# Optimization experiments

Measured on AMD Instinct MI355X. Metric: run time of the kernel, lower is better.

Reference implementation:

```python
import jax, jax.numpy as jnp
import numpy as np

GROUPS = 32
EPS = 1e-5
NUM_HEADS = 8


def group_norm(x, w, b):
    # x: (B, C, H, W)
    B, C, H, W = x.shape
    xg = x.reshape(B, GROUPS, C // GROUPS, H, W)
    mean = xg.mean(axis=(2, 3, 4), keepdims=True)
    var = xg.var(axis=(2, 3, 4), keepdims=True)
    xg = (xg - mean) * jax.lax.rsqrt(var + EPS)
    x = xg.reshape(B, C, H, W)
    return x * w[None, :, None, None] + b[None, :, None, None]


def setup_inputs() -> dict:
    key = jax.random.key(0)
    ks = jax.random.split(key, 4)
    B, C, H, W = 16, 512, 32, 32
    x = jax.random.normal(ks[0], (B, C, H, W), dtype=jnp.float32)
    gn_w = jnp.ones((C,), dtype=jnp.float32)
    gn_b = jnp.zeros((C,), dtype=jnp.float32)
    qkv_w = jax.random.normal(ks[1], (3 * C, C), dtype=jnp.float32) * 0.02  # 1x1 conv, no bias
    proj_w = jax.random.normal(ks[2], (C, C), dtype=jnp.float32) * 0.02     # 1x1 conv
    proj_b = jax.random.normal(ks[3], (C,), dtype=jnp.float32) * 0.02
    return {"x": x, "gn_w": gn_w, "gn_b": gn_b, "qkv_w": qkv_w,
            "proj_w": proj_w, "proj_b": proj_b}


def reference(x, gn_w, gn_b, qkv_w, proj_w, proj_b):
    B, C, H, W = x.shape
    heads = NUM_HEADS
    head_dim = C // heads
    HW = H * W
    scale = 1.0 / (head_dim ** 0.5)

    x = group_norm(x, gn_w, gn_b)  # residual uses the NORMED x, matching source

    qkv = jnp.einsum('bchw,oc->bohw', x, qkv_w)                     # (B, 3C, H, W)
    qkv = qkv.reshape(B, 3, heads, head_dim, HW)
    q, k, v = qkv[:, 0], qkv[:, 1], qkv[:, 2]                       # (B, heads, head_dim, HW)

    # Replicate the source's exact permute(0,2,3,1)+reshape (scrambles semantics, but faithful)
    def to_bmh(t):
        return jnp.transpose(t, (0, 2, 3, 1)).reshape(B * heads, HW, head_dim)
    q, k, v = to_bmh(q), to_bmh(k), to_bmh(v)

    attn = jax.nn.softmax(jnp.einsum('bnd,bmd->bnm', q, k) * scale, axis=-1)  # (B*heads, HW, HW)
    h = jnp.einsum('bnm,bmd->bnd', attn, v)                                   # (B*heads, HW, head_dim)

    h = h.reshape(B, heads, H, W, head_dim)
    h = jnp.transpose(h, (0, 1, 4, 2, 3)).reshape(B, C, H, W)

    out = jnp.einsum('bchw,oc->bohw', h, proj_w) + proj_b[None, :, None, None]
    return out + x
```

## Files before the change

kernel.cpp:

```cpp
#include <hip/hip_runtime.h>
#include <stdint.h>

typedef unsigned short u16;
typedef short bfrag __attribute__((ext_vector_type(8)));
typedef float ffrag __attribute__((ext_vector_type(4)));
typedef u16 us4 __attribute__((ext_vector_type(4)));
typedef uint32_t u32x4 __attribute__((ext_vector_type(4)));

#define HW 1024
#define C_DIM 512
#define O3 1536
#define BATCH 16

__device__ __forceinline__ u16 f2bf(float f) {
    uint32_t u = __builtin_bit_cast(uint32_t, f);
    u += 0x7FFFu + ((u >> 16) & 1u);
    return (u16)(u >> 16);
}
__device__ __forceinline__ float bf2f(u16 v) {
    return __builtin_bit_cast(float, (uint32_t)v << 16);
}
__device__ __forceinline__ float fexp2(float x) { return __builtin_amdgcn_exp2f(x); }
__device__ __forceinline__ void async16(const u16* src, u16* ldsDst) {
    __builtin_amdgcn_global_load_lds(
        (const __attribute__((address_space(1))) uint32_t*)src,
        (__attribute__((address_space(3))) uint32_t*)ldsDst, 16, 0, 0);
}

__global__ __launch_bounds__(256) void gn_cvt_kernel(
    const float* __restrict__ x, const float* __restrict__ gw, const float* __restrict__ gb,
    u16* __restrict__ xgt,
    const float* __restrict__ qkvw, u16* __restrict__ qkvwb,
    const float* __restrict__ projw, u16* __restrict__ projwb)
{
    __shared__ u16 tile[16 * 1032];
    __shared__ float red[8];
    const int tid = threadIdx.x;
    if (blockIdx.x >= 512) {
        int i = (blockIdx.x - 512) * 256 + tid;
        if (i < 196608) {
            float4 v = ((const float4*)qkvw)[i];
            us4 o = { f2bf(v.x), f2bf(v.y), f2bf(v.z), f2bf(v.w) };
            ((us4*)qkvwb)[i] = o;
        } else {
            int j = i - 196608;
            float4 v = ((const float4*)projw)[j];
            us4 o = { f2bf(v.x), f2bf(v.y), f2bf(v.z), f2bf(v.w) };
            ((us4*)projwb)[j] = o;
        }
        return;
    }
    const int batch = blockIdx.x >> 5, g = blockIdx.x & 31;
    const float* xp = x + ((size_t)batch * C_DIM + g * 16) * HW;

    float s = 0.f, ss = 0.f;
#pragma unroll
    for (int it = 0; it < 16; ++it) {
        int i4 = it * 256 + tid;
        float4 v = ((const float4*)xp)[i4];
        int ci = i4 >> 8;
        int hw = (i4 & 255) * 4;
        s += v.x + v.y + v.z + v.w;
        ss += v.x * v.x + v.y * v.y + v.z * v.z + v.w * v.w;
        us4 u = { f2bf(v.x), f2bf(v.y), f2bf(v.z), f2bf(v.w) };
        *(us4*)&tile[ci * 1032 + hw] = u;
    }
#pragma unroll
    for (int m = 1; m <= 32; m <<= 1) { s += __shfl_xor(s, m, 64); ss += __shfl_xor(ss, m, 64); }
    if ((tid & 63) == 0) { red[tid >> 6] = s; red[4 + (tid >> 6)] = ss; }
    __syncthreads();
    float S = red[0] + red[1] + red[2] + red[3];
    float SS = red[4] + red[5] + red[6] + red[7];
    const float mean = S * (1.f / 16384.f);
    const float istd = rsqrtf(SS * (1.f / 16384.f) - mean * mean + 1e-5f);

    u16* xtp = xgt + (size_t)batch * HW * C_DIM + g * 16;
#pragma unroll
    for (int it = 0; it < 16; ++it) {
        int hw = (tid >> 2) + it * 64;
        int c0 = (tid & 3) * 4;
        us4 o;
#pragma unroll
        for (int k2 = 0; k2 < 4; ++k2) {
            int ci = c0 + k2;
            float sc = gw[g * 16 + ci] * istd;
            float bi = gb[g * 16 + ci] - mean * sc;
            o[k2] = f2bf(bf2f(tile[ci * 1032 + hw]) * sc + bi);
        }
        *(us4*)&xtp[(size_t)hw * C_DIM + c0] = o;
    }
}

__global__ __launch_bounds__(256) void qkv_gemm_kernel(
    const u16* __restrict__ A, const u16* __restrict__ B, u16* __restrict__ Out,
    u16* __restrict__ vtout)
{
    __shared__ __align__(16) u16 smem[32768];
    const int tid = threadIdx.x;
    const int l = tid & 63, w = tid >> 6;
    const int swz = (blockIdx.x & 7) * 192 + (blockIdx.x >> 3);
    const int batch = swz / 96, t = swz % 96;
    const int tm = t / 12, tn = t % 12;
    A += (size_t)batch * (HW * C_DIM) + (size_t)tm * 128 * 512;
    B += (size_t)tn * 128 * 512;

    auto stage = [&](const u16* gbase, u16* lds, int kt) {
#pragma unroll
        for (int i = 0; i < 4; ++i) {
            int L = i * 256 + tid;
            int row = L >> 3, cs = L & 7;
            int c = cs ^ (row & 7);
            async16(gbase + (size_t)row * 512 + kt * 64 + c * 8,
                    lds + (size_t)(i * 256 + (tid & 192)) * 8);
        }
    };

    ffrag acc[4][4] = {};
    stage(A, smem, 0); stage(B, smem + 16384, 0);
    const int wr = (w >> 1) * 64, wc = (w & 1) * 64;
#pragma unroll
    for (int kt = 0; kt < 8; ++kt) {
        const int cur = kt & 1;
        asm volatile("s_waitcnt vmcnt(0)" ::: "memory");
        __builtin_amdgcn_s_barrier();
        __builtin_amdgcn_sched_barrier(0);
        if (kt < 7) {
            stage(A, smem + (cur ^ 1) * 8192, kt + 1);
            stage(B, smem + 16384 + (cur ^ 1) * 8192, kt + 1);
        }
        const u16* As = smem + cur * 8192;
        const u16* Bs = smem + 16384 + cur * 8192;
#pragma unroll
        for (int kc = 0; kc < 2; ++kc) {
            bfrag a[4], bb[4];
#pragma unroll
            for (int i = 0; i < 4; ++i) {
                int row = wr + i * 16 + (l & 15);
                int ch = (kc * 4 + (l >> 4)) ^ (row & 7);
                a[i] = *(const bfrag*)&As[row * 64 + ch * 8];
                int col = wc + i * 16 + (l & 15);
                int ch2 = (kc * 4 + (l >> 4)) ^ (col & 7);
                bb[i] = *(const bfrag*)&Bs[col * 64 + ch2 * 8];
            }
            __builtin_amdgcn_s_setprio(1);
#pragma unroll
            for (int i = 0; i < 4; ++i)
#pragma unroll
                for (int j = 0; j < 4; ++j)
                    acc[i][j] = __builtin_amdgcn_mfma_f32_16x16x32_bf16(a[i], bb[j], acc[i][j], 0, 0, 0);
            __builtin_amdgcn_s_setprio(0);
        }
    }
    __syncthreads();
    const int rbase = tm * 128 + wr + ((l >> 4) << 2);
    const int cbase = tn * 128 + wc + (l & 15);
    if (tn < 8) {
        u16* outp = Out + (size_t)batch * (HW * O3);
#pragma unroll
        for (int i = 0; i < 4; ++i)
#pragma unroll
            for (int j = 0; j < 4; ++j)
#pragma unroll
                for (int r = 0; r < 4; ++r)
                    outp[(size_t)(rbase + i * 16 + r) * O3 + cbase + j * 16] = f2bf(acc[i][j][r]);
    } else {
        u16* vb = vtout + (size_t)batch * 8 * 64 * HW;
        const int hd0 = tn * 128 - 1024;
#pragma unroll
        for (int i = 0; i < 4; ++i)
#pragma unroll
            for (int j = 0; j < 4; ++j) {
                int hd_l = wc + (l & 15) + j * 16;
                int m_l = wr + i * 16 + ((l >> 4) << 2);
                int s_l = (m_l & 96) | ((m_l & 12) << 1) | ((m_l & 16) >> 2);
                int c4 = s_l >> 2;
                int c4s = c4 ^ (hd_l & 7);
                us4 pk = { f2bf(acc[i][j][0]), f2bf(acc[i][j][1]),
                           f2bf(acc[i][j][2]), f2bf(acc[i][j][3]) };
                *(us4*)&smem[hd_l * 128 + c4s * 4] = pk;
            }
        __syncthreads();
#pragma unroll
        for (int it = 0; it < 16; ++it) {
            int f4 = it * 256 + tid;
            int hd_l = f4 >> 5, c4 = f4 & 31;
            int c4s = c4 ^ (hd_l & 7);
            us4 v = *(const us4*)&smem[hd_l * 128 + c4s * 4];
            *(us4*)&vb[(size_t)(hd0 + hd_l) * HW + tm * 128 + c4 * 4] = v;
        }
    }
}

__global__ __launch_bounds__(256) void proj_gemm_kernel(
    const u16* __restrict__ A, const u16* __restrict__ B, float* __restrict__ Out,
    const float* __restrict__ bias, const u16* __restrict__ residT)
{
    __shared__ __align__(16) u16 smem[24576];
    const int tid = threadIdx.x;
    const int l = tid & 63, w = tid >> 6;
    const int swz = (blockIdx.x & 7) * 64 + (blockIdx.x >> 3);
    const int batch = swz / 32, t = swz % 32;
    const int tm = t / 8, tn = t % 8;
    A += (size_t)tm * 128 * 512;
    B += (size_t)batch * (HW * C_DIM) + (size_t)tn * 128 * 512;

    auto stage = [&](const u16* gbase, u16* lds, int kt) {
#pragma unroll
        for (int i = 0; i < 2; ++i) {
            int L = i * 256 + tid;
            int row = L >> 2, cs = L & 3;
            int c = cs ^ ((row & 3) ^ ((row >> 2) & 3));
            async16(gbase + (size_t)row * 512 + kt * 32 + c * 8,
                    lds + (size_t)(i * 256 + (tid & 192)) * 8);
        }
    };

    ffrag acc[4][4] = {};
    stage(A, smem, 0);        stage(B, smem + 12288, 0);
    stage(A, smem + 4096, 1); stage(B, smem + 16384, 1);
    const int wr = (w >> 1) * 64, wc = (w & 1) * 64;
#pragma unroll
    for (int kt = 0; kt < 16; ++kt) {
        const int cur = kt % 3;
        if (kt < 15) asm volatile("s_waitcnt vmcnt(4)" ::: "memory");
        else         asm volatile("s_waitcnt vmcnt(0)" ::: "memory");
        __builtin_amdgcn_s_barrier();
        __builtin_amdgcn_sched_barrier(0);
        if (kt < 14) {
            int nxt = (kt + 2) % 3;
            stage(A, smem + nxt * 4096, kt + 2);
            stage(B, smem + 12288 + nxt * 4096, kt + 2);
        }
        const u16* As = smem + cur * 4096;
        const u16* Bs = smem + 12288 + cur * 4096;
        bfrag a[4], bb[4];
#pragma unroll
        for (int i = 0; i < 4; ++i) {
            int row = wr + i * 16 + (l & 15);
            int ch = (l >> 4) ^ ((row & 3) ^ ((row >> 2) & 3));
            a[i] = *(const bfrag*)&As[row * 32 + ch * 8];
            int col = wc + i * 16 + (l & 15);
            int ch2 = (l >> 4) ^ ((col & 3) ^ ((col >> 2) & 3));
            bb[i] = *(const bfrag*)&Bs[col * 32 + ch2 * 8];
        }
        __builtin_amdgcn_s_setprio(1);
#pragma unroll
        for (int i = 0; i < 4; ++i)
#pragma unroll
            for (int j = 0; j < 4; ++j)
                acc[i][j] = __builtin_amdgcn_mfma_f32_16x16x32_bf16(a[i], bb[j], acc[i][j], 0, 0, 0);
        __builtin_amdgcn_s_setprio(0);
    }
    const int rbase = tm * 128 + wr + ((l >> 4) << 2);
    const int cbase = tn * 128 + wc + (l & 15);
    float* outp = Out + (size_t)batch * (C_DIM * HW);
    const u16* rt = residT + (size_t)batch * (HW * C_DIM);
#pragma unroll
    for (int i = 0; i < 4; ++i)
#pragma unroll
        for (int j = 0; j < 4; ++j) {
            int cc = cbase + j * 16;
            us4 rv = *(const us4*)&rt[(size_t)cc * C_DIM + rbase + i * 16];
#pragma unroll
            for (int r = 0; r < 4; ++r) {
                int rr = rbase + i * 16 + r;
                outp[(size_t)rr * HW + cc] = acc[i][j][r] + bias[rr] + bf2f(rv[r]);
            }
        }
}

__global__ __launch_bounds__(512, 4) void attn_kernel(const u16* __restrict__ qkvt,
                                                      const u16* __restrict__ vt,
                                                      u16* __restrict__ ht)
{
    __shared__ __align__(16) u16 KVs[6 * 4096];
    const int tid = threadIdx.x, l = tid & 63, w = tid >> 6, g = l >> 4;
    const int swz = ((blockIdx.x & 7) << 6) + (blockIdx.x >> 3);
    const int nt = swz & 3, h = (swz >> 2) & 7, batch = swz >> 5;
    const u16* Qb = qkvt + (size_t)batch * HW * O3 + h * 64;
    const u16* Kb = Qb + 512;
    const u16* Vtb = vt + (size_t)(batch * 8 + h) * 64 * HW;
    const int n0 = nt * 256 + w * 32;
    const float cexp = 0.125f * 1.44269504f;

    bfrag qf[2][2];
#pragma unroll
    for (int ni = 0; ni < 2; ++ni)
#pragma unroll
        for (int kc = 0; kc < 2; ++kc)
            qf[ni][kc] = *(const bfrag*)&Qb[(size_t)(n0 + ni * 16 + (l & 15)) * O3 + kc * 32 + g * 8];

    bfrag ones;
#pragma unroll
    for (int k = 0; k < 8; ++k) ones[k] = (short)0x3F80;

    auto stageK = [&](int ms, u16* lds) {
        int row = tid >> 3, c = (tid & 7) ^ (row & 7);
        async16(&Kb[(size_t)(ms * 64 + row) * O3 + c * 8], lds + (size_t)(tid & 448) * 8);
    };
    auto stageV = [&](int ms, u16* lds) {
        int row = tid >> 3, c = (tid & 7) ^ (row & 7);
        async16(&Vtb[(size_t)row * HW + ms * 64 + c * 8], lds + (size_t)(tid & 448) * 8);
    };

    ffrag hacc[2][4] = {};
    ffrag accl[2] = {};

    stageK(0, KVs);        stageV(0, KVs + 3 * 4096);
    stageK(1, KVs + 4096); stageV(1, KVs + 4 * 4096);

#pragma unroll
    for (int ms = 0; ms < 16; ++ms) {
        const int cur = ms % 3;
        const u16* Ksc = KVs + cur * 4096;
        const u16* Vsc = KVs + (3 + cur) * 4096;
        if (ms < 15) asm volatile("s_waitcnt vmcnt(2)" ::: "memory");
        else         asm volatile("s_waitcnt vmcnt(0)" ::: "memory");
        __builtin_amdgcn_s_barrier();
        __builtin_amdgcn_sched_barrier(0);
        if (ms < 14) {
            int nxt = (ms + 2) % 3;
            stageK(ms + 2, KVs + nxt * 4096);
            stageV(ms + 2, KVs + (3 + nxt) * 4096);
        }

        ffrag s[2][4] = {};
        __builtin_amdgcn_s_setprio(1);
#pragma unroll
        for (int mj = 0; mj < 4; ++mj)
#pragma unroll
            for (int kc = 0; kc < 2; ++kc) {
                int m = mj * 16 + (l & 15);
                int ch = (kc * 4 + g) ^ (m & 7);
                bfrag kf = *(const bfrag*)&Ksc[m * 64 + ch * 8];
#pragma unroll
                for (int ni = 0; ni < 2; ++ni)
                    s[ni][mj] = __builtin_amdgcn_mfma_f32_16x16x32_bf16(kf, qf[ni][kc], s[ni][mj], 0, 0, 0);
            }
        __builtin_amdgcn_s_setprio(0);

        u32x4 pk[2][2];
#pragma unroll
        for (int ni = 0; ni < 2; ++ni)
#pragma unroll
            for (int kc = 0; kc < 2; ++kc)
#pragma unroll
                for (int hh = 0; hh < 2; ++hh) {
                    int mj = kc * 2 + hh;
                    float p0 = fexp2(s[ni][mj][0] * cexp);
                    float p1 = fexp2(s[ni][mj][1] * cexp);
                    float p2 = fexp2(s[ni][mj][2] * cexp);
                    float p3 = fexp2(s[ni][mj][3] * cexp);
                    pk[ni][kc][hh * 2] = __builtin_amdgcn_perm(
                        __builtin_bit_cast(uint32_t, p1), __builtin_bit_cast(uint32_t, p0), 0x07060302u);
                    pk[ni][kc][hh * 2 + 1] = __builtin_amdgcn_perm(
                        __builtin_bit_cast(uint32_t, p3), __builtin_bit_cast(uint32_t, p2), 0x07060302u);
                }

        __builtin_amdgcn_s_setprio(1);
#pragma unroll
        for (int kc = 0; kc < 2; ++kc) {
            bfrag pf0 = __builtin_bit_cast(bfrag, pk[0][kc]);
            bfrag pf1 = __builtin_bit_cast(bfrag, pk[1][kc]);
            accl[0] = __builtin_amdgcn_mfma_f32_16x16x32_bf16(pf0, ones, accl[0], 0, 0, 0);
            accl[1] = __builtin_amdgcn_mfma_f32_16x16x32_bf16(pf1, ones, accl[1], 0, 0, 0);
#pragma unroll
            for (int dj = 0; dj < 4; ++dj) {
                int d = dj * 16 + (l & 15);
                int ch = (kc * 4 + g) ^ (d & 7);
                bfrag vf = *(const bfrag*)&Vsc[d * 64 + ch * 8];
                hacc[0][dj] = __builtin_amdgcn_mfma_f32_16x16x32_bf16(pf0, vf, hacc[0][dj], 0, 0, 0);
                hacc[1][dj] = __builtin_amdgcn_mfma_f32_16x16x32_bf16(pf1, vf, hacc[1][dj], 0, 0, 0);
            }
        }
        __builtin_amdgcn_s_setprio(0);
    }

    u16* hp = ht + (size_t)batch * HW * C_DIM + h * 64;
#pragma unroll
    for (int ni = 0; ni < 2; ++ni) {
        float linv[4];
#pragma unroll
        for (int r = 0; r < 4; ++r) linv[r] = __builtin_amdgcn_rcpf(accl[ni][r]);
#pragma unroll
        for (int dj = 0; dj < 4; ++dj)
#pragma unroll
            for (int r = 0; r < 4; ++r) {
                int n = n0 + ni * 16 + g * 4 + r;
                int d = dj * 16 + (l & 15);
                hp[(size_t)n * C_DIM + d] = f2bf(hacc[ni][dj][r] * linv[r]);
            }
    }
}

extern "C" void kernel_launch(void* const* d_in, const int* in_sizes, int n_in,
                              void* d_out, int out_size, void* d_ws, size_t ws_size,
                              hipStream_t stream)
{
    const float* x = (const float*)d_in[0];
    const float* gw = (const float*)d_in[1];
    const float* gb = (const float*)d_in[2];
    const float* qkvw = (const float*)d_in[3];
    const float* projw = (const float*)d_in[4];
    const float* projb = (const float*)d_in[5];
    float* out = (float*)d_out;
    char* ws = (char*)d_ws;
    u16* ht    = (u16*)(ws);
    u16* xgt   = (u16*)(ws + 16777216);
    u16* qkvt  = (u16*)(ws + 33554432);
    u16* vt    = (u16*)(ws + 83886080);
    u16* qkvwb = (u16*)(ws + 100663296);
    u16* projwb= (u16*)(ws + 102236160);

    gn_cvt_kernel<<<1536, 256, 0, stream>>>(x, gw, gb, xgt, qkvw, qkvwb, projw, projwb);
    qkv_gemm_kernel<<<1536, 256, 0, stream>>>(xgt, qkvwb, qkvt, vt);
    attn_kernel<<<512, 512, 0, stream>>>(qkvt, vt, ht);
    proj_gemm_kernel<<<512, 256, 0, stream>>>(projwb, ht, out, projb, xgt);
}
```

Before: 103.7 us.

## Double-buffer with wider K stages in proj GEMM and attention loops

The projection GEMM moves from a 3-stage ring with K=32 tiles to a 2-stage double buffer with K=64 tiles and an 8-way XOR swizzle. This halves the barrier count per output tile. The attention kernel now loads two 64-key tiles per barrier into a 4-slot ring, so it synchronizes half as often. Both waits become vmcnt(0), which removes the partial overlap of the deeper pipeline and raises LDS use (64KB in attention), so occupancy may drop.

```diff
diff --git a/kernel.cpp b/kernel.cpp
--- a/kernel.cpp
+++ b/kernel.cpp
@@ -195,7 +195,7 @@
     const u16* __restrict__ A, const u16* __restrict__ B, float* __restrict__ Out,
     const float* __restrict__ bias, const u16* __restrict__ residT)
 {
-    __shared__ __align__(16) u16 smem[24576];
+    __shared__ __align__(16) u16 smem[32768];
     const int tid = threadIdx.x;
     const int l = tid & 63, w = tid >> 6;
     const int swz = (blockIdx.x & 7) * 64 + (blockIdx.x >> 3);
@@ -206,50 +206,50 @@
 
     auto stage = [&](const u16* gbase, u16* lds, int kt) {
 #pragma unroll
-        for (int i = 0; i < 2; ++i) {
+        for (int i = 0; i < 4; ++i) {
             int L = i * 256 + tid;
-            int row = L >> 2, cs = L & 3;
-            int c = cs ^ ((row & 3) ^ ((row >> 2) & 3));
-            async16(gbase + (size_t)row * 512 + kt * 32 + c * 8,
+            int row = L >> 3, cs = L & 7;
+            int c = cs ^ (row & 7);
+            async16(gbase + (size_t)row * 512 + kt * 64 + c * 8,
                     lds + (size_t)(i * 256 + (tid & 192)) * 8);
         }
     };
 
     ffrag acc[4][4] = {};
-    stage(A, smem, 0);        stage(B, smem + 12288, 0);
-    stage(A, smem + 4096, 1); stage(B, smem + 16384, 1);
+    stage(A, smem, 0); stage(B, smem + 16384, 0);
     const int wr = (w >> 1) * 64, wc = (w & 1) * 64;
 #pragma unroll
-    for (int kt = 0; kt < 16; ++kt) {
-        const int cur = kt % 3;
-        if (kt < 15) asm volatile("s_waitcnt vmcnt(4)" ::: "memory");
-        else         asm volatile("s_waitcnt vmcnt(0)" ::: "memory");
+    for (int kt = 0; kt < 8; ++kt) {
+        const int cur = kt & 1;
+        asm volatile("s_waitcnt vmcnt(0)" ::: "memory");
         __builtin_amdgcn_s_barrier();
         __builtin_amdgcn_sched_barrier(0);
-        if (kt < 14) {
-            int nxt = (kt + 2) % 3;
-            stage(A, smem + nxt * 4096, kt + 2);
-            stage(B, smem + 12288 + nxt * 4096, kt + 2);
-        }
-        const u16* As = smem + cur * 4096;
-        const u16* Bs = smem + 12288 + cur * 4096;
-        bfrag a[4], bb[4];
-#pragma unroll
-        for (int i = 0; i < 4; ++i) {
-            int row = wr + i * 16 + (l & 15);
-            int ch = (l >> 4) ^ ((row & 3) ^ ((row >> 2) & 3));
-            a[i] = *(const bfrag*)&As[row * 32 + ch * 8];
-            int col = wc + i * 16 + (l & 15);
-            int ch2 = (l >> 4) ^ ((col & 3) ^ ((col >> 2) & 3));
-            bb[i] = *(const bfrag*)&Bs[col * 32 + ch2 * 8];
-        }
-        __builtin_amdgcn_s_setprio(1);
-#pragma unroll
-        for (int i = 0; i < 4; ++i)
-#pragma unroll
-            for (int j = 0; j < 4; ++j)
-                acc[i][j] = __builtin_amdgcn_mfma_f32_16x16x32_bf16(a[i], bb[j], acc[i][j], 0, 0, 0);
-        __builtin_amdgcn_s_setprio(0);
+        if (kt < 7) {
+            stage(A, smem + (cur ^ 1) * 8192, kt + 1);
+            stage(B, smem + 16384 + (cur ^ 1) * 8192, kt + 1);
+        }
+        const u16* As = smem + cur * 8192;
+        const u16* Bs = smem + 16384 + cur * 8192;
+#pragma unroll
+        for (int kc = 0; kc < 2; ++kc) {
+            bfrag a[4], bb[4];
+#pragma unroll
+            for (int i = 0; i < 4; ++i) {
+                int row = wr + i * 16 + (l & 15);
+                int ch = (kc * 4 + (l >> 4)) ^ (row & 7);
+                a[i] = *(const bfrag*)&As[row * 64 + ch * 8];
+                int col = wc + i * 16 + (l & 15);
+                int ch2 = (kc * 4 + (l >> 4)) ^ (col & 7);
+                bb[i] = *(const bfrag*)&Bs[col * 64 + ch2 * 8];
+            }
+            __builtin_amdgcn_s_setprio(1);
+#pragma unroll
+            for (int i = 0; i < 4; ++i)
+#pragma unroll
+                for (int j = 0; j < 4; ++j)
+                    acc[i][j] = __builtin_amdgcn_mfma_f32_16x16x32_bf16(a[i], bb[j], acc[i][j], 0, 0, 0);
+            __builtin_amdgcn_s_setprio(0);
+        }
     }
     const int rbase = tm * 128 + wr + ((l >> 4) << 2);
     const int cbase = tn * 128 + wc + (l & 15);
@@ -273,7 +273,7 @@
                                                       const u16* __restrict__ vt,
                                                       u16* __restrict__ ht)
 {
-    __shared__ __align__(16) u16 KVs[6 * 4096];
+    __shared__ __align__(16) u16 KVs[8 * 4096];
     const int tid = threadIdx.x, l = tid & 63, w = tid >> 6, g = l >> 4;
     const int swz = ((blockIdx.x & 7) << 6) + (blockIdx.x >> 3);
     const int nt = swz & 3, h = (swz >> 2) & 7, batch = swz >> 5;
@@ -306,74 +306,78 @@
     ffrag hacc[2][4] = {};
     ffrag accl[2] = {};
 
-    stageK(0, KVs);        stageV(0, KVs + 3 * 4096);
-    stageK(1, KVs + 4096); stageV(1, KVs + 4 * 4096);
-
-#pragma unroll
-    for (int ms = 0; ms < 16; ++ms) {
-        const int cur = ms % 3;
-        const u16* Ksc = KVs + cur * 4096;
-        const u16* Vsc = KVs + (3 + cur) * 4096;
-        if (ms < 15) asm volatile("s_waitcnt vmcnt(2)" ::: "memory");
-        else         asm volatile("s_waitcnt vmcnt(0)" ::: "memory");
+    stageK(0, KVs);        stageV(0, KVs + 4 * 4096);
+    stageK(1, KVs + 4096); stageV(1, KVs + 5 * 4096);
+
+#pragma unroll
+    for (int st = 0; st < 8; ++st) {
+        asm volatile("s_waitcnt vmcnt(0)" ::: "memory");
         __builtin_amdgcn_s_barrier();
         __builtin_amdgcn_sched_barrier(0);
-        if (ms < 14) {
-            int nxt = (ms + 2) % 3;
-            stageK(ms + 2, KVs + nxt * 4096);
-            stageV(ms + 2, KVs + (3 + nxt) * 4096);
-        }
-
-        ffrag s[2][4] = {};
-        __builtin_amdgcn_s_setprio(1);
-#pragma unroll
-        for (int mj = 0; mj < 4; ++mj)
+        if (st < 7) {
+            const int mt2 = 2 * st + 2, mt3 = 2 * st + 3;
+            stageK(mt2, KVs + (mt2 & 3) * 4096);
+            stageV(mt2, KVs + (4 + (mt2 & 3)) * 4096);
+            stageK(mt3, KVs + (mt3 & 3) * 4096);
+            stageV(mt3, KVs + (4 + (mt3 & 3)) * 4096);
+        }
+#pragma unroll
+        for (int half = 0; half < 2; ++half) {
+            const int mt = 2 * st + half;
+            const u16* Ksc = KVs + (mt & 3) * 4096;
+            const u16* Vsc = KVs + (4 + (mt & 3)) * 4096;
+
+            ffrag s[2][4] = {};
+            __builtin_amdgcn_s_setprio(1);
+#pragma unroll
+            for (int mj = 0; mj < 4; ++mj)
+#pragma unroll
+                for (int kc = 0; kc < 2; ++kc) {
+                    int m = mj * 16 + (l & 15);
+                    int ch = (kc * 4 + g) ^ (m & 7);
+                    bfrag kf = *(const bfrag*)&Ksc[m * 64 + ch * 8];
+#pragma unroll
+                    for (int ni = 0; ni < 2; ++ni)
+                        s[ni][mj] = __builtin_amdgcn_mfma_f32_16x16x32_bf16(kf, qf[ni][kc], s[ni][mj], 0, 0, 0);
+                }
+            __builtin_amdgcn_s_setprio(0);
+
+            u32x4 pk[2][2];
+#pragma unroll
+            for (int ni = 0; ni < 2; ++ni)
+#pragma unroll
+                for (int kc = 0; kc < 2; ++kc)
+#pragma unroll
+                    for (int hh = 0; hh < 2; ++hh) {
+                        int mj = kc * 2 + hh;
+                        float p0 = fexp2(s[ni][mj][0] * cexp);
+                        float p1 = fexp2(s[ni][mj][1] * cexp);
+                        float p2 = fexp2(s[ni][mj][2] * cexp);
+                        float p3 = fexp2(s[ni][mj][3] * cexp);
+                        pk[ni][kc][hh * 2] = __builtin_amdgcn_perm(
+                            __builtin_bit_cast(uint32_t, p1), __builtin_bit_cast(uint32_t, p0), 0x07060302u);
+                        pk[ni][kc][hh * 2 + 1] = __builtin_amdgcn_perm(
+                            __builtin_bit_cast(uint32_t, p3), __builtin_bit_cast(uint32_t, p2), 0x07060302u);
+                    }
+
+            __builtin_amdgcn_s_setprio(1);
 #pragma unroll
             for (int kc = 0; kc < 2; ++kc) {
-                int m = mj * 16 + (l & 15);
-                int ch = (kc * 4 + g) ^ (m & 7);
-                bfrag kf = *(const bfrag*)&Ksc[m * 64 + ch * 8];
-#pragma unroll
-                for (int ni = 0; ni < 2; ++ni)
-                    s[ni][mj] = __builtin_amdgcn_mfma_f32_16x16x32_bf16(kf, qf[ni][kc], s[ni][mj], 0, 0, 0);
-            }
-        __builtin_amdgcn_s_setprio(0);
-
-        u32x4 pk[2][2];
-#pragma unroll
-        for (int ni = 0; ni < 2; ++ni)
-#pragma unroll
-            for (int kc = 0; kc < 2; ++kc)
-#pragma unroll
-                for (int hh = 0; hh < 2; ++hh) {
-                    int mj = kc * 2 + hh;
-                    float p0 = fexp2(s[ni][mj][0] * cexp);
-                    float p1 = fexp2(s[ni][mj][1] * cexp);
-                    float p2 = fexp2(s[ni][mj][2] * cexp);
-                    float p3 = fexp2(s[ni][mj][3] * cexp);
-                    pk[ni][kc][hh * 2] = __builtin_amdgcn_perm(
-                        __builtin_bit_cast(uint32_t, p1), __builtin_bit_cast(uint32_t, p0), 0x07060302u);
-                    pk[ni][kc][hh * 2 + 1] = __builtin_amdgcn_perm(
-                        __builtin_bit_cast(uint32_t, p3), __builtin_bit_cast(uint32_t, p2), 0x07060302u);
+                bfrag pf0 = __builtin_bit_cast(bfrag, pk[0][kc]);
+                bfrag pf1 = __builtin_bit_cast(bfrag, pk[1][kc]);
+                accl[0] = __builtin_amdgcn_mfma_f32_16x16x32_bf16(pf0, ones, accl[0], 0, 0, 0);
+                accl[1] = __builtin_amdgcn_mfma_f32_16x16x32_bf16(pf1, ones, accl[1], 0, 0, 0);
+#pragma unroll
+                for (int dj = 0; dj < 4; ++dj) {
+                    int d = dj * 16 + (l & 15);
+                    int ch = (kc * 4 + g) ^ (d & 7);
+                    bfrag vf = *(const bfrag*)&Vsc[d * 64 + ch * 8];
+                    hacc[0][dj] = __builtin_amdgcn_mfma_f32_16x16x32_bf16(pf0, vf, hacc[0][dj], 0, 0, 0);
+                    hacc[1][dj] = __builtin_amdgcn_mfma_f32_16x16x32_bf16(pf1, vf, hacc[1][dj], 0, 0, 0);
                 }
-
-        __builtin_amdgcn_s_setprio(1);
-#pragma unroll
-        for (int kc = 0; kc < 2; ++kc) {
-            bfrag pf0 = __builtin_bit_cast(bfrag, pk[0][kc]);
-            bfrag pf1 = __builtin_bit_cast(bfrag, pk[1][kc]);
-            accl[0] = __builtin_amdgcn_mfma_f32_16x16x32_bf16(pf0, ones, accl[0], 0, 0, 0);
-            accl[1] = __builtin_amdgcn_mfma_f32_16x16x32_bf16(pf1, ones, accl[1], 0, 0, 0);
-#pragma unroll
-            for (int dj = 0; dj < 4; ++dj) {
-                int d = dj * 16 + (l & 15);
-                int ch = (kc * 4 + g) ^ (d & 7);
-                bfrag vf = *(const bfrag*)&Vsc[d * 64 + ch * 8];
-                hacc[0][dj] = __builtin_amdgcn_mfma_f32_16x16x32_bf16(pf0, vf, hacc[0][dj], 0, 0, 0);
-                hacc[1][dj] = __builtin_amdgcn_mfma_f32_16x16x32_bf16(pf1, vf, hacc[1][dj], 0, 0, 0);
-            }
-        }
-        __builtin_amdgcn_s_setprio(0);
+            }
+            __builtin_amdgcn_s_setprio(0);
+        }
     }
 
     u16* hp = ht + (size_t)batch * HW * C_DIM + h * 64;
```

Result: no change. 103.4 us (-0.4%).
